# Optimization experiments

Measured on AMD Instinct MI355X. Metric: run time of the kernel, lower is better.

Reference implementation:

```python
import jax, jax.numpy as jnp
import numpy as np

B, C, H, W = 16, 512, 64, 64
L, D = 77, 768
NH = 8
HD = C // NH
EPS = 1e-5


def layernorm(x, g, b):
    m = jnp.mean(x, axis=-1, keepdims=True)
    v = jnp.var(x, axis=-1, keepdims=True)
    return (x - m) * jax.lax.rsqrt(v + EPS) * g + b


def setup_inputs() -> dict:
    key = jax.random.key(0)
    ks = jax.random.split(key, 12)
    s_c = 1.0 / np.sqrt(C)
    s_d = 1.0 / np.sqrt(D)
    return {
        "x": jax.random.normal(ks[0], (B, C, H, W), jnp.float32),
        "text_features": jax.random.normal(ks[1], (B, L, D), jnp.float32),
        "wq": jax.random.normal(ks[2], (C, C), jnp.float32) * s_c,
        "bq": jnp.zeros((C,), jnp.float32),
        "wk": jax.random.normal(ks[3], (C, D), jnp.float32) * s_d,
        "bk": jnp.zeros((C,), jnp.float32),
        "wv": jax.random.normal(ks[4], (C, D), jnp.float32) * s_d,
        "bv": jnp.zeros((C,), jnp.float32),
        "wo": jax.random.normal(ks[5], (C, C), jnp.float32) * s_c,
        "bo": jnp.zeros((C,), jnp.float32),
        "g1": jnp.ones((C,), jnp.float32),
        "b1": jnp.zeros((C,), jnp.float32),
        "g2": jnp.ones((C,), jnp.float32),
        "b2": jnp.zeros((C,), jnp.float32),
    }


def reference(x, text_features, wq, bq, wk, bk, wv, bv, wo, bo, g1, b1, g2, b2):
    b, c, h, w = x.shape
    # 1x1 conv query projection
    q = jnp.einsum('bchw,oc->bohw', x, wq) + bq[None, :, None, None]
    # 2D positional encoding: first c/2 channels vary along w, next c/2 along h
    pos_x = jnp.broadcast_to(jnp.linspace(0.0, 1.0, w)[None, :], (h, w))
    pos_y = jnp.broadcast_to(jnp.linspace(0.0, 1.0, h)[:, None], (h, w))
    pe = jnp.concatenate([
        jnp.broadcast_to(pos_x[None], (c // 2, h, w)),
        jnp.broadcast_to(pos_y[None], (c // 2, h, w)),
    ], axis=0)  # [C,H,W]
    q = q + 0.05 * pe[None]
    # flatten spatial -> tokens, layernorm over channels
    q_flat = q.reshape(b, c, h * w).transpose(0, 2, 1)  # [B,HW,C]
    q_norm = layernorm(q_flat, g1, b1)
    qh = q_norm.reshape(b, h * w, NH, HD)  # [B,HW,NH,HD]
    # text key/value projections
    k = jnp.einsum('bld,cd->blc', text_features, wk) + bk
    v = jnp.einsum('bld,cd->blc', text_features, wv) + bv
    k_norm = layernorm(k, g2, b2)
    kh = k_norm.reshape(b, -1, NH, HD)
    vh = v.reshape(b, -1, NH, HD)
    scale = HD ** -0.5
    attn = jnp.einsum('bqhd,bkhd->bhqk', qh, kh) * scale  # [B,NH,HW,L]
    attn = jax.nn.softmax(attn, axis=-1)  # dropout is identity in eval
    out = jnp.einsum('bhqk,bkhd->bqhd', attn, vh).reshape(b, h * w, c)
    out = out.transpose(0, 2, 1).reshape(b, c, h, w)
    out = jnp.einsum('bchw,oc->bohw', out, wo) + bo[None, :, None, None]
    return out + x
```

## Files before the change

kernel.cpp:

```cpp
#include <hip/hip_runtime.h>
#include <stdint.h>

#define BD   16
#define CD   512
#define HD_  64
#define NH_  8
#define HWD  4096
#define LD   77
#define DD   768

typedef __bf16 bf16;
typedef bf16 bf16x8 __attribute__((ext_vector_type(8)));
typedef float f32x4 __attribute__((ext_vector_type(4)));

__device__ __forceinline__ void async16(const bf16* g, bf16* l) {
  __builtin_amdgcn_global_load_lds(
      (const __attribute__((address_space(1))) void*)g,
      (__attribute__((address_space(3))) void*)l, 16, 0, 0);
}

__device__ __forceinline__ unsigned short bfb(float f) {
  bf16 h = (bf16)f;
  return __builtin_bit_cast(unsigned short, h);
}

__global__ __launch_bounds__(256) void xpose_cvt(const float* __restrict__ X,
                                                 bf16* __restrict__ Y) {
  __shared__ float tile[64][68];
  const int b = blockIdx.z, c0 = blockIdx.y * 64, t0 = blockIdx.x * 64;
  const int tid = threadIdx.x;
  const float* Xb = X + ((size_t)b * CD + c0) * HWD + t0;
#pragma unroll
  for (int p = 0; p < 4; ++p) {
    int c = (tid >> 4) + p * 16;
    int t = (tid & 15) * 4;
    float4 v = *(const float4*)(Xb + (size_t)c * HWD + t);
    *(float4*)&tile[c][t] = v;
  }
  __syncthreads();
  int t = tid >> 2, cb = (tid & 3) * 16;
  union { uint4 u[2]; unsigned short us[16]; } pk;
#pragma unroll
  for (int j = 0; j < 16; ++j) pk.us[j] = bfb(tile[cb + j][t]);
  uint4* Yp = (uint4*)(Y + ((size_t)(b * HWD + t0 + t)) * CD + c0 + cb);
  Yp[0] = pk.u[0];
  Yp[1] = pk.u[1];
}

__global__ void cvt_bf16_k(const float* __restrict__ X, bf16* __restrict__ Y, int n) {
  int i = (blockIdx.x * 256 + threadIdx.x) * 8;
  if (i >= n) return;
  float4 a = *(const float4*)(X + i);
  float4 c = *(const float4*)(X + i + 4);
  union { uint4 u; unsigned short us[8]; } pk;
  pk.us[0] = bfb(a.x); pk.us[1] = bfb(a.y); pk.us[2] = bfb(a.z); pk.us[3] = bfb(a.w);
  pk.us[4] = bfb(c.x); pk.us[5] = bfb(c.y); pk.us[6] = bfb(c.z); pk.us[7] = bfb(c.w);
  *(uint4*)(Y + i) = pk.u;
}

template <int TM, int TN, int MODE>
__global__ __launch_bounds__(256)
void gemm_bt(const bf16* __restrict__ A, const bf16* __restrict__ B,
             int M, int N, int K,
             const float* __restrict__ bias, const float* __restrict__ xres,
             float* __restrict__ D) {
  constexpr int WM = TM / 2, WN = TN / 2;
  constexpr int AFR = WM / 16, BFR = WN / 16;
  constexpr int ACH = TM / 8, TCH = (TM + TN) / 8, WCH = TCH / 4;
  __shared__ bf16 sA[TM * 64];
  __shared__ bf16 sB[TN * 64];
  const int tid = threadIdx.x, wave = tid >> 6, lane = tid & 63;
  const int m0 = blockIdx.y * TM, n0 = blockIdx.x * TN;
  const int wm = (wave >> 1) * WM, wn = (wave & 1) * WN;
  const int sub = lane >> 3, col8 = (lane & 7) * 8;
  const int mlo = lane & 15, khi = lane >> 4;
  f32x4 acc[AFR][BFR] = {};

  for (int k0 = 0; k0 < K; k0 += 64) {
#pragma unroll
    for (int r = 0; r < WCH; ++r) {
      int ci = wave * WCH + r;
      if (ci < ACH) {
        int row = ci * 8 + sub;
        int g = m0 + row;
        if (g > M - 1) g = M - 1;
        async16(A + (size_t)g * K + k0 + col8, &sA[ci * 512]);
      } else {
        int cj = ci - ACH;
        int row = cj * 8 + sub;
        async16(B + (size_t)(n0 + row) * K + k0 + col8, &sB[cj * 512]);
      }
    }
    __syncthreads();
#pragma unroll
    for (int kc = 0; kc < 2; ++kc) {
      bf16x8 af[AFR], bfv[BFR];
      const int ko = kc * 32 + khi * 8;
#pragma unroll
      for (int i = 0; i < AFR; ++i)
        af[i] = *(const bf16x8*)&sA[(wm + i * 16 + mlo) * 64 + ko];
#pragma unroll
      for (int j = 0; j < BFR; ++j)
        bfv[j] = *(const bf16x8*)&sB[(wn + j * 16 + mlo) * 64 + ko];
#pragma unroll
      for (int i = 0; i < AFR; ++i)
#pragma unroll
        for (int j = 0; j < BFR; ++j)
          acc[i][j] = __builtin_amdgcn_mfma_f32_16x16x32_bf16(af[i], bfv[j],
                                                              acc[i][j], 0, 0, 0);
    }
    __syncthreads();
  }

#pragma unroll
  for (int i = 0; i < AFR; ++i) {
    const int mb = m0 + wm + i * 16 + khi * 4;
#pragma unroll
    for (int j = 0; j < BFR; ++j) {
      const int n = n0 + wn + j * 16 + mlo;
#pragma unroll
      for (int r = 0; r < 4; ++r) {
        const int m = mb + r;
        float val = acc[i][j][r];
        if constexpr (MODE == 1) {
          if (m < M) D[(size_t)m * CD + n] = val + bias[n];
        } else {
          int b = n >> 12, hw = n & (HWD - 1);
          size_t addr = ((size_t)(b * CD + m)) * HWD + hw;
          D[addr] = val + bias[m] + xres[addr];
        }
      }
    }
  }
}

__global__ __launch_bounds__(256) void qgemm_ln(const bf16* __restrict__ A,
                                                const bf16* __restrict__ Bw,
                                                const float* __restrict__ bias,
                                                const float* __restrict__ g1,
                                                const float* __restrict__ b1,
                                                bf16* __restrict__ Y) {
  constexpr int TM = 64, KK = 512;
  constexpr int AFR = 4, BFR = 8;
  __shared__ bf16 sA[TM * 64];
  __shared__ bf16 sB[512 * 64];
  __shared__ float sStat[4][TM][2];
  const int tid = threadIdx.x, wave = tid >> 6, lane = tid & 63;
  const int m0 = blockIdx.x * TM;
  const int wn = wave * 128;
  const int sub = lane >> 3, col8 = (lane & 7) * 8;
  const int mlo = lane & 15, khi = lane >> 4;
  f32x4 acc[AFR][BFR] = {};

  for (int k0 = 0; k0 < KK; k0 += 64) {
#pragma unroll
    for (int r = 0; r < 18; ++r) {
      int ci = wave * 18 + r;
      if (ci < 8) {
        int row = ci * 8 + sub;
        async16(A + (size_t)(m0 + row) * KK + k0 + col8, &sA[ci * 512]);
      } else {
        int cj = ci - 8;
        int row = cj * 8 + sub;
        async16(Bw + (size_t)row * KK + k0 + col8, &sB[cj * 512]);
      }
    }
    __syncthreads();
#pragma unroll
    for (int kc = 0; kc < 2; ++kc) {
      const int ko = kc * 32 + khi * 8;
      bf16x8 af[AFR], bfv[BFR];
#pragma unroll
      for (int i = 0; i < AFR; ++i)
        af[i] = *(const bf16x8*)&sA[(i * 16 + mlo) * 64 + ko];
#pragma unroll
      for (int j = 0; j < BFR; ++j)
        bfv[j] = *(const bf16x8*)&sB[(wn + j * 16 + mlo) * 64 + ko];
#pragma unroll
      for (int i = 0; i < AFR; ++i)
#pragma unroll
        for (int j = 0; j < BFR; ++j)
          acc[i][j] = __builtin_amdgcn_mfma_f32_16x16x32_bf16(af[i], bfv[j],
                                                              acc[i][j], 0, 0, 0);
    }
    __syncthreads();
  }

  float cb[8], cg[8], ct[8];
#pragma unroll
  for (int j = 0; j < 8; ++j) {
    int n = wn + j * 16 + mlo;
    cb[j] = bias[n];
    cg[j] = g1[n];
    ct[j] = b1[n];
  }

#pragma unroll
  for (int i = 0; i < AFR; ++i) {
#pragma unroll
    for (int r = 0; r < 4; ++r) {
      const int row = i * 16 + khi * 4 + r;
      const int hw = (m0 + row) & (HWD - 1);
      const float pex = (float)(hw & 63) * (0.05f / 63.0f);
      const float pey = (float)(hw >> 6) * (0.05f / 63.0f);
      float s = 0.f, sq = 0.f;
#pragma unroll
      for (int j = 0; j < 8; ++j) {
        float v = acc[i][j][r] + cb[j] + ((wn + j * 16) < 256 ? pex : pey);
        acc[i][j][r] = v;
        s += v;
        sq += v * v;
      }
      s += __shfl_xor(s, 1);  sq += __shfl_xor(sq, 1);
      s += __shfl_xor(s, 2);  sq += __shfl_xor(sq, 2);
      s += __shfl_xor(s, 4);  sq += __shfl_xor(sq, 4);
      s += __shfl_xor(s, 8);  sq += __shfl_xor(sq, 8);
      if (mlo == 0) {
        sStat[wave][row][0] = s;
        sStat[wave][row][1] = sq;
      }
    }
  }
  __syncthreads();

#pragma unroll
  for (int i = 0; i < AFR; ++i) {
#pragma unroll
    for (int r = 0; r < 4; ++r) {
      const int row = i * 16 + khi * 4 + r;
      float s = sStat[0][row][0] + sStat[1][row][0] +
                sStat[2][row][0] + sStat[3][row][0];
      float sq = sStat[0][row][1] + sStat[1][row][1] +
                 sStat[2][row][1] + sStat[3][row][1];
      float mean = s * (1.0f / 512.0f);
      float var = sq * (1.0f / 512.0f) - mean * mean;
      float rstd = rsqrtf(var + 1e-5f);
      bf16* yr = Y + (size_t)(m0 + row) * CD + wn + mlo;
#pragma unroll
      for (int j = 0; j < 8; ++j)
        yr[j * 16] = (bf16)((acc[i][j][r] - mean) * rstd * cg[j] + ct[j]);
    }
  }
}

__global__ __launch_bounds__(256) void ln_rows(const float* __restrict__ X,
                                               const float* __restrict__ gg,
                                               const float* __restrict__ bb,
                                               bf16* __restrict__ Y, int nrows,
                                               int khlayout) {
  const int wv = threadIdx.x >> 6, lane = threadIdx.x & 63;
  const int row = blockIdx.x * 4 + wv;
  if (row >= nrows) return;
  const float* xr = X + (size_t)row * CD + lane * 8;
  float4 v0 = *(const float4*)xr;
  float4 v1 = *(const float4*)(xr + 4);
  float xv[8] = {v0.x, v0.y, v0.z, v0.w, v1.x, v1.y, v1.z, v1.w};
  float s = 0.f, sq = 0.f;
#pragma unroll
  for (int j = 0; j < 8; ++j) { s += xv[j]; sq += xv[j] * xv[j]; }
#pragma unroll
  for (int off = 1; off < 64; off <<= 1) {
    s += __shfl_xor(s, off);
    sq += __shfl_xor(sq, off);
  }
  float mean = s * (1.0f / 512.0f);
  float var = sq * (1.0f / 512.0f) - mean * mean;
  float rstd = rsqrtf(var + 1e-5f);
  const int c0 = lane * 8;
  union { uint4 u; unsigned short us[8]; } pk;
#pragma unroll
  for (int j = 0; j < 8; ++j)
    pk.us[j] = bfb((xv[j] - mean) * rstd * gg[c0 + j] + bb[c0 + j]);
  size_t ya;
  if (khlayout) {
    int bq = row / LD, l = row - bq * LD;
    int hh = lane >> 3, dd = (lane & 7) * 8;
    ya = (((size_t)(bq * NH_ + hh)) * LD + l) * HD_ + dd;
  } else {
    ya = (size_t)row * CD + c0;
  }
  *(uint4*)(Y + ya) = pk.u;
}

__global__ __launch_bounds__(256) void make_vt(const float* __restrict__ vraw,
                                               bf16* __restrict__ vt) {
  const int bh = blockIdx.x, b = bh >> 3, h = bh & 7;
  const int tid = threadIdx.x, d = tid & 63, lg = tid >> 6;
  for (int l = lg; l < 96; l += 4) {
    float v = 0.f;
    if (l < LD) v = vraw[((size_t)(b * LD + l)) * CD + h * HD_ + d];
    vt[((size_t)(bh * HD_ + d)) * 96 + l] = (bf16)v;
  }
}

__global__ __launch_bounds__(256) void attn_k(const bf16* __restrict__ Q,
                                              const bf16* __restrict__ KH,
                                              const bf16* __restrict__ VT,
                                              bf16* __restrict__ O) {
  __shared__ bf16 P[4][16 * 104];
  const int tid = threadIdx.x, wv = tid >> 6, lane = tid & 63;
  const int m = lane & 15, kg = lane >> 4;
  const int q0 = blockIdx.x * 64, h = blockIdx.y, b = blockIdx.z;
  const int bh = b * NH_ + h;

  const size_t qoff = ((size_t)(b * HWD + q0 + wv * 16 + m)) * CD + h * HD_;
  bf16x8 a0 = *(const bf16x8*)(Q + qoff + kg * 8);
  bf16x8 a1 = *(const bf16x8*)(Q + qoff + 32 + kg * 8);

  const bf16* Kb = KH + (size_t)bh * LD * HD_;
  f32x4 s[5];
#pragma unroll
  for (int kt = 0; kt < 5; ++kt) {
    int key = kt * 16 + m;
    if (key > LD - 1) key = LD - 1;
    const bf16* kr = Kb + key * HD_ + kg * 8;
    bf16x8 b0 = *(const bf16x8*)kr;
    bf16x8 b1 = *(const bf16x8*)(kr + 32);
    f32x4 z = {0.f, 0.f, 0.f, 0.f};
    z = __builtin_amdgcn_mfma_f32_16x16x32_bf16(a0, b0, z, 0, 0, 0);
    z = __builtin_amdgcn_mfma_f32_16x16x32_bf16(a1, b1, z, 0, 0, 0);
    s[kt] = z;
  }

  bf16* Pw = &P[wv][0];
#pragma unroll
  for (int r = 0; r < 4; ++r) {
    float sc[5];
#pragma unroll
    for (int kt = 0; kt < 5; ++kt) {
      float v = s[kt][r] * 0.125f;
      if (kt == 4 && m >= LD - 64) v = -3.0e38f;
      sc[kt] = v;
    }
    float mx = fmaxf(fmaxf(fmaxf(sc[0], sc[1]), fmaxf(sc[2], sc[3])), sc[4]);
    mx = fmaxf(mx, __shfl_xor(mx, 1));
    mx = fmaxf(mx, __shfl_xor(mx, 2));
    mx = fmaxf(mx, __shfl_xor(mx, 4));
    mx = fmaxf(mx, __shfl_xor(mx, 8));
    float sum = 0.f;
#pragma unroll
    for (int kt = 0; kt < 5; ++kt) {
      sc[kt] = __expf(sc[kt] - mx);
      sum += sc[kt];
    }
    sum += __shfl_xor(sum, 1);
    sum += __shfl_xor(sum, 2);
    sum += __shfl_xor(sum, 4);
    sum += __shfl_xor(sum, 8);
    float inv = 1.0f / sum;
    const int prow = kg * 4 + r;
#pragma unroll
    for (int kt = 0; kt < 5; ++kt)
      Pw[prow * 104 + kt * 16 + m] = (bf16)(sc[kt] * inv);
    Pw[prow * 104 + 80 + m] = (bf16)0.f;
  }
  __syncthreads();

  bf16x8 ap[3];
#pragma unroll
  for (int kc = 0; kc < 3; ++kc)
    ap[kc] = *(const bf16x8*)&Pw[m * 104 + kc * 32 + kg * 8];

  const bf16* Vb = VT + (size_t)bh * HD_ * 96;
  f32x4 o[4] = {};
#pragma unroll
  for (int nt = 0; nt < 4; ++nt) {
#pragma unroll
    for (int kc = 0; kc < 3; ++kc) {
      bf16x8 bv = *(const bf16x8*)(Vb + (nt * 16 + m) * 96 + kc * 32 + kg * 8);
      o[nt] = __builtin_amdgcn_mfma_f32_16x16x32_bf16(ap[kc], bv, o[nt], 0, 0, 0);
    }
  }
#pragma unroll
  for (int nt = 0; nt < 4; ++nt)
#pragma unroll
    for (int r = 0; r < 4; ++r) {
      const int row = b * HWD + q0 + wv * 16 + kg * 4 + r;
      O[(size_t)row * CD + h * HD_ + nt * 16 + m] = (bf16)(o[nt][r]);
    }
}

extern "C" void kernel_launch(void* const* d_in, const int* in_sizes, int n_in,
                              void* d_out, int out_size, void* d_ws, size_t ws_size,
                              hipStream_t stream) {
  const float* x    = (const float*)d_in[0];
  const float* text = (const float*)d_in[1];
  const float* wq   = (const float*)d_in[2];
  const float* bq   = (const float*)d_in[3];
  const float* wk   = (const float*)d_in[4];
  const float* bk   = (const float*)d_in[5];
  const float* wv   = (const float*)d_in[6];
  const float* bv   = (const float*)d_in[7];
  const float* wo   = (const float*)d_in[8];
  const float* bo   = (const float*)d_in[9];
  const float* g1   = (const float*)d_in[10];
  const float* b1   = (const float*)d_in[11];
  const float* g2   = (const float*)d_in[12];
  const float* b2   = (const float*)d_in[13];
  float* out = (float*)d_out;

  char* p = (char*)d_ws;
  auto alloc = [&](size_t bytes) {
    char* r = p;
    p += (bytes + 255) & ~(size_t)255;
    return r;
  };
  bf16* xt     = (bf16*)alloc((size_t)BD * HWD * CD * 2);
  bf16* attn_o = (bf16*)alloc((size_t)BD * HWD * CD * 2);
  bf16* textb  = (bf16*)alloc((size_t)BD * LD * DD * 2);
  bf16* wqb    = (bf16*)alloc((size_t)CD * CD * 2);
  bf16* wkb    = (bf16*)alloc((size_t)CD * DD * 2);
  bf16* wvb    = (bf16*)alloc((size_t)CD * DD * 2);
  bf16* wob    = (bf16*)alloc((size_t)CD * CD * 2);
  float* kraw  = (float*)alloc((size_t)BD * LD * CD * 4);
  float* vraw  = (float*)alloc((size_t)BD * LD * CD * 4);
  bf16* kh     = (bf16*)alloc((size_t)BD * NH_ * LD * HD_ * 2);
  bf16* vt     = (bf16*)alloc((size_t)BD * NH_ * HD_ * 96 * 2);
  bf16* qbf = (bf16*)out;

  xpose_cvt<<<dim3(HWD / 64, CD / 64, BD), 256, 0, stream>>>(x, xt);
  const int nt_ = BD * LD * DD;
  cvt_bf16_k<<<(nt_ / 8 + 255) / 256, 256, 0, stream>>>(text, textb, nt_);
  cvt_bf16_k<<<(CD * CD / 8 + 255) / 256, 256, 0, stream>>>(wq, wqb, CD * CD);
  cvt_bf16_k<<<(CD * DD / 8 + 255) / 256, 256, 0, stream>>>(wk, wkb, CD * DD);
  cvt_bf16_k<<<(CD * DD / 8 + 255) / 256, 256, 0, stream>>>(wv, wvb, CD * DD);
  cvt_bf16_k<<<(CD * CD / 8 + 255) / 256, 256, 0, stream>>>(wo, wob, CD * CD);

  gemm_bt<128, 128, 1><<<dim3(4, 10), 256, 0, stream>>>(
      textb, wkb, BD * LD, CD, DD, bk, nullptr, kraw);
  gemm_bt<128, 128, 1><<<dim3(4, 10), 256, 0, stream>>>(
      textb, wvb, BD * LD, CD, DD, bv, nullptr, vraw);
  ln_rows<<<(BD * LD + 3) / 4, 256, 0, stream>>>(kraw, g2, b2, kh, BD * LD, 1);
  make_vt<<<BD * NH_, 256, 0, stream>>>(vraw, vt);

  qgemm_ln<<<dim3(BD * HWD / 64), 256, 0, stream>>>(xt, wqb, bq, g1, b1, qbf);

  attn_k<<<dim3(HWD / 64, NH_, BD), 256, 0, stream>>>(qbf, kh, vt, attn_o);

  gemm_bt<256, 128, 3><<<dim3(512, 2), 256, 0, stream>>>(
      wob, attn_o, CD, BD * HWD, CD, bo, x, out);
}
```

Measured before the change: 611.1 us.

## Merge conversion launches, fuse K/V GEMMs, swap output GEMM operands for vector epilogue

Five separate fp32-to-bf16 conversion launches are replaced by one kernel that picks its source and destination from the block index. The K and V projection GEMMs become a single launch whose upper half of blocks switches to the V weights, bias and output. The output projection now uses tokens as the M dimension and weights as N, so the residual-add epilogue reads and writes float4 runs along the spatial axis. The aim is to cut launch overhead and improve the final GEMM's epilogue memory access, at the cost of extra parameters and a changed tile mapping in the largest GEMM.

```diff
diff --git a/kernel.cpp b/kernel.cpp
--- a/kernel.cpp
+++ b/kernel.cpp
@@ -47,15 +47,26 @@
   Yp[1] = pk.u[1];
 }
 
-__global__ void cvt_bf16_k(const float* __restrict__ X, bf16* __restrict__ Y, int n) {
-  int i = (blockIdx.x * 256 + threadIdx.x) * 8;
-  if (i >= n) return;
-  float4 a = *(const float4*)(X + i);
-  float4 c = *(const float4*)(X + i + 4);
+__global__ __launch_bounds__(256) void cvt_all(
+    const float* __restrict__ t, const float* __restrict__ q,
+    const float* __restrict__ k, const float* __restrict__ v,
+    const float* __restrict__ o, bf16* __restrict__ tb, bf16* __restrict__ qb,
+    bf16* __restrict__ kb, bf16* __restrict__ vb, bf16* __restrict__ ob) {
+  int bid = blockIdx.x;
+  const float* src;
+  bf16* dst;
+  if (bid < 462) { src = t; dst = tb; }
+  else if (bid < 590) { src = q; dst = qb; bid -= 462; }
+  else if (bid < 782) { src = k; dst = kb; bid -= 590; }
+  else if (bid < 974) { src = v; dst = vb; bid -= 782; }
+  else { src = o; dst = ob; bid -= 974; }
+  int i = (bid * 256 + threadIdx.x) * 8;
+  float4 a = *(const float4*)(src + i);
+  float4 c = *(const float4*)(src + i + 4);
   union { uint4 u; unsigned short us[8]; } pk;
   pk.us[0] = bfb(a.x); pk.us[1] = bfb(a.y); pk.us[2] = bfb(a.z); pk.us[3] = bfb(a.w);
   pk.us[4] = bfb(c.x); pk.us[5] = bfb(c.y); pk.us[6] = bfb(c.z); pk.us[7] = bfb(c.w);
-  *(uint4*)(Y + i) = pk.u;
+  *(uint4*)(dst + i) = pk.u;
 }
 
 template <int TM, int TN, int MODE>
@@ -63,14 +74,20 @@
 void gemm_bt(const bf16* __restrict__ A, const bf16* __restrict__ B,
              int M, int N, int K,
              const float* __restrict__ bias, const float* __restrict__ xres,
-             float* __restrict__ D) {
+             float* __restrict__ D,
+             const bf16* __restrict__ B2, const float* __restrict__ bias2,
+             float* __restrict__ D2) {
   constexpr int WM = TM / 2, WN = TN / 2;
   constexpr int AFR = WM / 16, BFR = WN / 16;
   constexpr int ACH = TM / 8, TCH = (TM + TN) / 8, WCH = TCH / 4;
   __shared__ bf16 sA[TM * 64];
   __shared__ bf16 sB[TN * 64];
   const int tid = threadIdx.x, wave = tid >> 6, lane = tid & 63;
-  const int m0 = blockIdx.y * TM, n0 = blockIdx.x * TN;
+  const int m0 = blockIdx.y * TM;
+  int n0 = blockIdx.x * TN;
+  if constexpr (MODE == 2) {
+    if (n0 >= (N >> 1)) { B = B2; bias = bias2; D = D2; n0 -= (N >> 1); }
+  }
   const int wm = (wave >> 1) * WM, wn = (wave & 1) * WN;
   const int sub = lane >> 3, col8 = (lane & 7) * 8;
   const int mlo = lane & 15, khi = lane >> 4;
@@ -112,22 +129,39 @@
     __syncthreads();
   }
 
-#pragma unroll
-  for (int i = 0; i < AFR; ++i) {
-    const int mb = m0 + wm + i * 16 + khi * 4;
-#pragma unroll
-    for (int j = 0; j < BFR; ++j) {
-      const int n = n0 + wn + j * 16 + mlo;
-#pragma unroll
-      for (int r = 0; r < 4; ++r) {
-        const int m = mb + r;
-        float val = acc[i][j][r];
-        if constexpr (MODE == 1) {
-          if (m < M) D[(size_t)m * CD + n] = val + bias[n];
-        } else {
-          int b = n >> 12, hw = n & (HWD - 1);
-          size_t addr = ((size_t)(b * CD + m)) * HWD + hw;
-          D[addr] = val + bias[m] + xres[addr];
+  if constexpr (MODE == 3) {
+    float bn[BFR];
+#pragma unroll
+    for (int j = 0; j < BFR; ++j) bn[j] = bias[n0 + wn + j * 16 + mlo];
+#pragma unroll
+    for (int i = 0; i < AFR; ++i) {
+      const int m = m0 + wm + i * 16 + khi * 4;
+      const int b = m >> 12, hw = m & (HWD - 1);
+      const float* xr0 = xres + ((size_t)b * CD) * HWD + hw;
+      float* d0 = D + ((size_t)b * CD) * HWD + hw;
+#pragma unroll
+      for (int j = 0; j < BFR; ++j) {
+        const size_t off = (size_t)(n0 + wn + j * 16 + mlo) * HWD;
+        float4 xr = *(const float4*)(xr0 + off);
+        float4 ov;
+        ov.x = acc[i][j][0] + bn[j] + xr.x;
+        ov.y = acc[i][j][1] + bn[j] + xr.y;
+        ov.z = acc[i][j][2] + bn[j] + xr.z;
+        ov.w = acc[i][j][3] + bn[j] + xr.w;
+        *(float4*)(d0 + off) = ov;
+      }
+    }
+  } else {
+#pragma unroll
+    for (int i = 0; i < AFR; ++i) {
+      const int mb = m0 + wm + i * 16 + khi * 4;
+#pragma unroll
+      for (int j = 0; j < BFR; ++j) {
+        const int n = n0 + wn + j * 16 + mlo;
+#pragma unroll
+        for (int r = 0; r < 4; ++r) {
+          const int m = mb + r;
+          if (m < M) D[(size_t)m * CD + n] = acc[i][j][r] + bias[n];
         }
       }
     }
@@ -419,17 +453,11 @@
   bf16* qbf = (bf16*)out;
 
   xpose_cvt<<<dim3(HWD / 64, CD / 64, BD), 256, 0, stream>>>(x, xt);
-  const int nt_ = BD * LD * DD;
-  cvt_bf16_k<<<(nt_ / 8 + 255) / 256, 256, 0, stream>>>(text, textb, nt_);
-  cvt_bf16_k<<<(CD * CD / 8 + 255) / 256, 256, 0, stream>>>(wq, wqb, CD * CD);
-  cvt_bf16_k<<<(CD * DD / 8 + 255) / 256, 256, 0, stream>>>(wk, wkb, CD * DD);
-  cvt_bf16_k<<<(CD * DD / 8 + 255) / 256, 256, 0, stream>>>(wv, wvb, CD * DD);
-  cvt_bf16_k<<<(CD * CD / 8 + 255) / 256, 256, 0, stream>>>(wo, wob, CD * CD);
-
-  gemm_bt<128, 128, 1><<<dim3(4, 10), 256, 0, stream>>>(
-      textb, wkb, BD * LD, CD, DD, bk, nullptr, kraw);
-  gemm_bt<128, 128, 1><<<dim3(4, 10), 256, 0, stream>>>(
-      textb, wvb, BD * LD, CD, DD, bv, nullptr, vraw);
+  cvt_all<<<1102, 256, 0, stream>>>(text, wq, wk, wv, wo,
+                                    textb, wqb, wkb, wvb, wob);
+
+  gemm_bt<128, 128, 2><<<dim3(8, 10), 256, 0, stream>>>(
+      textb, wkb, BD * LD, 2 * CD, DD, bk, nullptr, kraw, wvb, bv, vraw);
   ln_rows<<<(BD * LD + 3) / 4, 256, 0, stream>>>(kraw, g2, b2, kh, BD * LD, 1);
   make_vt<<<BD * NH_, 256, 0, stream>>>(vraw, vt);
 
@@ -437,6 +465,6 @@
 
   attn_k<<<dim3(HWD / 64, NH_, BD), 256, 0, stream>>>(qbf, kh, vt, attn_o);
 
-  gemm_bt<256, 128, 3><<<dim3(512, 2), 256, 0, stream>>>(
-      wob, attn_o, CD, BD * HWD, CD, bo, x, out);
-}
+  gemm_bt<256, 128, 3><<<dim3(CD / 128, BD * HWD / 256), 256, 0, stream>>>(
+      attn_o, wob, BD * HWD, CD, CD, bo, x, out, nullptr, nullptr, nullptr);
+}
```

Result: faster. 581.4 us (-4.9%).
